# Performance work log

Hardware: AMD Instinct MI355X
Metric: run time of the kernel (lower is better)

## Reference

```python
import jax, jax.numpy as jnp
import numpy as np
from jax import lax

M, T, WINDOW = 4096, 2048, 25
NEG_DIAG = -1e10  # matches alphas.fill_diagonal_(-1e10)


def setup_inputs() -> dict:
    key = jax.random.key(0)
    k_ys, k_a, k_r, k_b0, k_b1 = jax.random.split(key, 5)
    ys = jax.random.uniform(k_ys, (M, T), dtype=jnp.float32) * 10.0  # case counts
    alphas = 0.01 * jax.random.normal(k_a, (M, M), dtype=jnp.float32)
    repro = 1.0 + 0.01 * jax.random.normal(k_r, (M, WINDOW), dtype=jnp.float32)  # init ones
    b0 = 0.1 * jax.random.normal(k_b0, (M, 1), dtype=jnp.float32)
    b1 = 0.01 * jax.random.normal(k_b1, (M, 1), dtype=jnp.float32)
    t = jnp.arange(T, dtype=jnp.int32) + 1
    return {"ys": ys, "alphas": alphas, "repro": repro, "b0": b0, "b1": b1, "t": t}


def reference(ys, alphas, repro, b0, b1, t):
    m, _ = ys.shape
    window = repro.shape[1]
    offset = window - 1
    # metapopulation weights: sigmoid adjacency with diagonal forced to ~0
    diag = jnp.eye(m, dtype=bool)
    W = jax.nn.sigmoid(jnp.where(diag, jnp.asarray(NEG_DIAG, ys.dtype), alphas))
    # depthwise conv1d (cross-correlation), groups=M, VALID padding -> (M, T-window+1)
    Z = lax.conv_general_dilated(
        ys[None],                 # (1, M, T)
        repro[:, None, :],        # (M, 1, window)
        window_strides=(1,),
        padding='VALID',
        feature_group_count=m,
        dimension_numbers=('NCH', 'OIH', 'NCH'),
    )[0]                          # (M, T')
    ys_n = ys[:, offset:]         # (M, T')
    # beta_net: per-node softplus-linear in time -> (M, T), then narrow
    tt = t.astype(ys.dtype)
    beta = jax.nn.softplus(b0 + b1 * tt[None, :])[:, offset:]  # (M, T')
    return beta * (jax.nn.softplus(Z) + W @ ys_n)
```

## Files before the change

### kernel.cpp

```cpp
#include <hip/hip_runtime.h>
#include <stdint.h>

#define M_DIM 4096
#define T_DIM 2048
#define N_OUT 2024
#define N_PAD 2048
#define WIN   25
#define K_DIM 4096

typedef float f32x4 __attribute__((ext_vector_type(4)));

__device__ __forceinline__ unsigned short f2bf(float x) {
  unsigned u = __float_as_uint(x);
  u += 0x7FFF + ((u >> 16) & 1);
  return (unsigned short)(u >> 16);
}
__device__ __forceinline__ float bf2f(unsigned short h) {
  return __uint_as_float(((unsigned)h) << 16);
}

__device__ __forceinline__ void gl2lds16(const void* g, void* l) {
  __builtin_amdgcn_global_load_lds(
      (const __attribute__((address_space(1))) unsigned int*)g,
      (__attribute__((address_space(3))) unsigned int*)l, 16, 0, 0);
}

__device__ __forceinline__ int pk_fp8x4(float a, float b, float c, float d) {
  int w = __builtin_amdgcn_cvt_pk_fp8_f32(a, b, 0, false);
  w = __builtin_amdgcn_cvt_pk_fp8_f32(c, d, w, true);
  return w;
}

__global__ __launch_bounds__(256) void k_wcast(const float* __restrict__ alphas,
                                               unsigned char* __restrict__ W8) {
  size_t i8 = ((size_t)blockIdx.x * 256 + threadIdx.x) * 8;
  const float4 v0 = *(const float4*)(alphas + i8);
  const float4 v1 = *(const float4*)(alphas + i8 + 4);
  int row = (int)(i8 >> 12);
  int col = (int)(i8 & 4095);
  float a[8] = {v0.x, v0.y, v0.z, v0.w, v1.x, v1.y, v1.z, v1.w};
  float w[8];
#pragma unroll
  for (int j = 0; j < 8; ++j)
    w[j] = (row == col + j) ? 0.f : 1.f / (1.f + __expf(-a[j]));
  int p0 = pk_fp8x4(w[0], w[1], w[2], w[3]);
  int p1 = pk_fp8x4(w[4], w[5], w[6], w[7]);
  *(uint2*)(W8 + i8) = uint2{(unsigned)p0, (unsigned)p1};
}

__global__ __launch_bounds__(256) void k_convT(const float* __restrict__ ys,
                                               const float* __restrict__ repro,
                                               unsigned short* __restrict__ Sbf,
                                               unsigned char* __restrict__ BT8) {
  __shared__ float sy[32][284];
  __shared__ float sr[32][26];
  const int tid = threadIdx.x;
  const int c0 = blockIdx.x * 256;
  const int m0 = blockIdx.y * 32;

  for (int slot = tid; slot < 32 * 70; slot += 256) {
    int r = slot / 70, f = slot % 70;
    int c = c0 + f * 4;
    float4 v = (c < T_DIM) ? *(const float4*)(ys + (size_t)(m0 + r) * T_DIM + c)
                           : float4{0.f, 0.f, 0.f, 0.f};
    sy[r][f * 4 + 0] = v.x; sy[r][f * 4 + 1] = v.y;
    sy[r][f * 4 + 2] = v.z; sy[r][f * 4 + 3] = v.w;
  }
  for (int slot = tid; slot < 32 * WIN; slot += 256) {
    int r = slot / WIN, k = slot % WIN;
    sr[r][k] = repro[(m0 + r) * WIN + k];
  }
  __syncthreads();

  {
    const int r = tid >> 3;
    const int cbase = (tid & 7) * 32;
    float y[56];
#pragma unroll
    for (int i = 0; i < 56; ++i) y[i] = sy[r][cbase + i];
    float rv[WIN];
#pragma unroll
    for (int k = 0; k < WIN; ++k) rv[k] = sr[r][k];
    unsigned pk[16];
#pragma unroll
    for (int jj = 0; jj < 32; ++jj) {
      float z = 0.f;
#pragma unroll
      for (int k = 0; k < WIN; ++k) z += y[jj + k] * rv[k];
      float sp = fmaxf(z, 0.f) + log1pf(__expf(-fabsf(z)));
      int gj = c0 + cbase + jj;
      unsigned short h = (gj < N_OUT) ? f2bf(sp) : (unsigned short)0;
      if (jj & 1) pk[jj >> 1] |= ((unsigned)h) << 16;
      else        pk[jj >> 1]  = (unsigned)h;
    }
    unsigned short* dst = Sbf + (size_t)(m0 + r) * N_PAD + c0 + cbase;
    *(uint4*)(dst)      = *(const uint4*)(pk + 0);
    *(uint4*)(dst + 8)  = *(const uint4*)(pk + 4);
    *(uint4*)(dst + 16) = *(const uint4*)(pk + 8);
    *(uint4*)(dst + 24) = *(const uint4*)(pk + 12);
  }

  {
    const int n = c0 + tid;
    const bool ok = (n < N_OUT);
    unsigned w[8];
#pragma unroll
    for (int i = 0; i < 8; ++i) {
      float a0 = ok ? sy[4 * i + 0][tid + 24] : 0.f;
      float a1 = ok ? sy[4 * i + 1][tid + 24] : 0.f;
      float a2 = ok ? sy[4 * i + 2][tid + 24] : 0.f;
      float a3 = ok ? sy[4 * i + 3][tid + 24] : 0.f;
      w[i] = (unsigned)pk_fp8x4(a0, a1, a2, a3);
    }
    unsigned char* dst = BT8 + (size_t)n * K_DIM + m0;
    *(uint4*)(dst)      = uint4{w[0], w[1], w[2], w[3]};
    *(uint4*)(dst + 16) = uint4{w[4], w[5], w[6], w[7]};
  }
}

__global__ __launch_bounds__(512, 4) void k_gemm(const unsigned char* __restrict__ W8,
                                                 const unsigned char* __restrict__ BT8,
                                                 const unsigned short* __restrict__ Sbf,
                                                 const float* __restrict__ b0,
                                                 const float* __restrict__ b1,
                                                 float* __restrict__ out) {
  __shared__ __align__(64) unsigned char lA[4][128 * 64];
  __shared__ __align__(64) unsigned char lB[4][128 * 64];
  const int tid  = threadIdx.x;
  const int wave = tid >> 6;
  const int lane = tid & 63;
  const int wm = wave >> 2;
  const int wn = wave & 3;
  const int m16  = lane & 15;
  const int quad = lane >> 4;

  const int fid  = blockIdx.y * gridDim.x + blockIdx.x;
  const int swz  = (fid & 7) * 64 + (fid >> 3);
  const int tileN = (swz & 15) * 128;
  const int tileM = (swz >> 4) * 128;

  const int key  = (m16 >> 1) & 3;
  const int sub  = (quad & 1) * 8;
  const int rowA = (wm * 64 + m16) * 64;
  const int rowB = (wn * 32 + m16) * 64;
  int hOf[2];
#pragma unroll
  for (int h = 0; h < 2; ++h)
    hOf[h] = (((2 * h + (quad >> 1)) ^ key) << 4) + sub;

  const int o = wave * 1024 + lane * 16;
  const int r = o >> 6;
  const int s = (o >> 4) & 3;
  const int q = s ^ ((r >> 1) & 3);
  const unsigned char* gA = W8  + (size_t)(tileM + r) * K_DIM + q * 16;
  const unsigned char* gB = BT8 + (size_t)(tileN + r) * K_DIM + q * 16;
  const int ldsOff = wave * 1024;

  f32x4 acc[4][2];
#pragma unroll
  for (int i = 0; i < 4; ++i)
#pragma unroll
    for (int j = 0; j < 2; ++j) acc[i][j] = f32x4{0.f, 0.f, 0.f, 0.f};

  auto stage = [&](int buf, int kt_) {
    const size_t kb_ = (size_t)kt_ * 64;
    gl2lds16(gA + kb_, &lA[buf][ldsOff]);
    gl2lds16(gB + kb_, &lB[buf][ldsOff]);
  };
  auto compute = [&](int buf) {
#pragma unroll
    for (int h = 0; h < 2; ++h) {
      long long aF[4], bF[2];
#pragma unroll
      for (int i = 0; i < 4; ++i)
        aF[i] = *(const long long*)&lA[buf][rowA + i * 1024 + hOf[h]];
#pragma unroll
      for (int j = 0; j < 2; ++j)
        bF[j] = *(const long long*)&lB[buf][rowB + j * 1024 + hOf[h]];
#pragma unroll
      for (int i = 0; i < 4; ++i)
#pragma unroll
        for (int j = 0; j < 2; ++j)
          acc[i][j] = __builtin_amdgcn_mfma_f32_16x16x32_fp8_fp8(
              aF[i], bF[j], acc[i][j], 0, 0, 0);
    }
  };

  stage(0, 0);
  stage(1, 1);
  stage(2, 2);

#pragma unroll 1
  for (int kt = 0; kt < K_DIM / 64; kt += 4) {
    stage(3, kt + 3);
    asm volatile("s_waitcnt vmcnt(6)" ::: "memory");
    __builtin_amdgcn_s_barrier();
    asm volatile("" ::: "memory");
    compute(0);
    __builtin_amdgcn_s_barrier();
    asm volatile("" ::: "memory");

    if (kt + 4 < K_DIM / 64) {
      stage(0, kt + 4);
      asm volatile("s_waitcnt vmcnt(6)" ::: "memory");
    } else {
      asm volatile("s_waitcnt vmcnt(4)" ::: "memory");
    }
    __builtin_amdgcn_s_barrier();
    asm volatile("" ::: "memory");
    compute(1);
    __builtin_amdgcn_s_barrier();
    asm volatile("" ::: "memory");

    if (kt + 5 < K_DIM / 64) {
      stage(1, kt + 5);
      asm volatile("s_waitcnt vmcnt(6)" ::: "memory");
    } else {
      asm volatile("s_waitcnt vmcnt(2)" ::: "memory");
    }
    __builtin_amdgcn_s_barrier();
    asm volatile("" ::: "memory");
    compute(2);
    __builtin_amdgcn_s_barrier();
    asm volatile("" ::: "memory");

    if (kt + 6 < K_DIM / 64) {
      stage(2, kt + 6);
      asm volatile("s_waitcnt vmcnt(6)" ::: "memory");
    } else {
      asm volatile("s_waitcnt vmcnt(0)" ::: "memory");
    }
    __builtin_amdgcn_s_barrier();
    asm volatile("" ::: "memory");
    compute(3);
    __builtin_amdgcn_s_barrier();
    asm volatile("" ::: "memory");
  }

#pragma unroll
  for (int j = 0; j < 2; ++j) {
    int gn = tileN + wn * 32 + j * 16 + m16;
    if (gn >= N_OUT) continue;
    float tval = (float)(gn + WIN);
#pragma unroll
    for (int i = 0; i < 4; ++i) {
#pragma unroll
      for (int r2 = 0; r2 < 4; ++r2) {
        int gm = tileM + wm * 64 + i * 16 + quad * 4 + r2;
        float x = b0[gm] + b1[gm] * tval;
        float beta = fmaxf(x, 0.f) + log1pf(__expf(-fabsf(x)));
        float sv = bf2f(Sbf[(size_t)gm * N_PAD + gn]);
        out[(size_t)gm * N_OUT + gn] = beta * (sv + acc[i][j][r2]);
      }
    }
  }
}

extern "C" void kernel_launch(void* const* d_in, const int* in_sizes, int n_in,
                              void* d_out, int out_size, void* d_ws, size_t ws_size,
                              hipStream_t stream) {
  const float* ys     = (const float*)d_in[0];
  const float* alphas = (const float*)d_in[1];
  const float* repro  = (const float*)d_in[2];
  const float* b0     = (const float*)d_in[3];
  const float* b1     = (const float*)d_in[4];
  float* out = (float*)d_out;

  char* ws = (char*)d_ws;
  unsigned char*  W8  = (unsigned char*)ws;
  unsigned char*  BT8 = (unsigned char*)(ws + (size_t)M_DIM * K_DIM);
  unsigned short* Sbf = (unsigned short*)(ws + (size_t)M_DIM * K_DIM
                                             + (size_t)N_PAD * K_DIM);

  k_wcast<<<(M_DIM * (size_t)K_DIM) / 8 / 256, 256, 0, stream>>>(alphas, W8);
  k_convT<<<dim3(T_DIM / 256, M_DIM / 32), 256, 0, stream>>>(ys, repro, Sbf, BT8);
  k_gemm<<<dim3(N_PAD / 128, M_DIM / 128), 512, 0, stream>>>(W8, BT8, Sbf,
                                                             b0, b1, out);
}
```

Baseline: 253.9 us.

## Enlarge FP8 GEMM tile to 256x128 with 1024-thread blocks and double buffering

```diff
diff --git a/kernel.cpp b/kernel.cpp
--- a/kernel.cpp
+++ b/kernel.cpp
@@ -118,14 +118,14 @@
   }
 }
 
-__global__ __launch_bounds__(512, 4) void k_gemm(const unsigned char* __restrict__ W8,
-                                                 const unsigned char* __restrict__ BT8,
-                                                 const unsigned short* __restrict__ Sbf,
-                                                 const float* __restrict__ b0,
-                                                 const float* __restrict__ b1,
-                                                 float* __restrict__ out) {
-  __shared__ __align__(64) unsigned char lA[4][128 * 64];
-  __shared__ __align__(64) unsigned char lB[4][128 * 64];
+__global__ __launch_bounds__(1024, 4) void k_gemm(const unsigned char* __restrict__ W8,
+                                                  const unsigned char* __restrict__ BT8,
+                                                  const unsigned short* __restrict__ Sbf,
+                                                  const float* __restrict__ b0,
+                                                  const float* __restrict__ b1,
+                                                  float* __restrict__ out) {
+  __shared__ __align__(64) unsigned char lA[2][256 * 64];
+  __shared__ __align__(64) unsigned char lB[2][128 * 64];
   const int tid  = threadIdx.x;
   const int wave = tid >> 6;
   const int lane = tid & 63;
@@ -135,9 +135,9 @@
   const int quad = lane >> 4;
 
   const int fid  = blockIdx.y * gridDim.x + blockIdx.x;
-  const int swz  = (fid & 7) * 64 + (fid >> 3);
+  const int swz  = (fid & 7) * 32 + (fid >> 3);
   const int tileN = (swz & 15) * 128;
-  const int tileM = (swz >> 4) * 128;
+  const int tileM = (swz >> 4) * 256;
 
   const int key  = (m16 >> 1) & 3;
   const int sub  = (quad & 1) * 8;
@@ -148,13 +148,15 @@
   for (int h = 0; h < 2; ++h)
     hOf[h] = (((2 * h + (quad >> 1)) ^ key) << 4) + sub;
 
-  const int o = wave * 1024 + lane * 16;
-  const int r = o >> 6;
-  const int s = (o >> 4) & 3;
-  const int q = s ^ ((r >> 1) & 3);
-  const unsigned char* gA = W8  + (size_t)(tileM + r) * K_DIM + q * 16;
-  const unsigned char* gB = BT8 + (size_t)(tileN + r) * K_DIM + q * 16;
-  const int ldsOff = wave * 1024;
+  const int oA = tid * 16;
+  const int rA = oA >> 6;
+  const int sA = (oA >> 4) & 3;
+  const int qA = sA ^ ((rA >> 1) & 3);
+  const unsigned char* gA = W8 + (size_t)(tileM + rA) * K_DIM + qA * 16;
+  const int rB = (tid * 16) >> 6;
+  const int qB = (((tid * 16) >> 4) & 3) ^ ((rB >> 1) & 3);
+  const unsigned char* gB = BT8 + (size_t)(tileN + rB) * K_DIM + qB * 16;
+  const int ldsBase = wave * 1024;
 
   f32x4 acc[4][2];
 #pragma unroll
@@ -164,8 +166,8 @@
 
   auto stage = [&](int buf, int kt_) {
     const size_t kb_ = (size_t)kt_ * 64;
-    gl2lds16(gA + kb_, &lA[buf][ldsOff]);
-    gl2lds16(gB + kb_, &lB[buf][ldsOff]);
+    gl2lds16(gA + kb_, &lA[buf][ldsBase]);
+    if (wave < 8) gl2lds16(gB + kb_, &lB[buf][ldsBase]);
   };
   auto compute = [&](int buf) {
 #pragma unroll
@@ -187,52 +189,34 @@
   };
 
   stage(0, 0);
-  stage(1, 1);
-  stage(2, 2);
 
 #pragma unroll 1
-  for (int kt = 0; kt < K_DIM / 64; kt += 4) {
-    stage(3, kt + 3);
-    asm volatile("s_waitcnt vmcnt(6)" ::: "memory");
+  for (int kt = 0; kt < K_DIM / 64; kt += 2) {
+    stage(1, kt + 1);
+    if (wave < 8) {
+      asm volatile("s_waitcnt vmcnt(2)" ::: "memory");
+    } else {
+      asm volatile("s_waitcnt vmcnt(1)" ::: "memory");
+    }
     __builtin_amdgcn_s_barrier();
     asm volatile("" ::: "memory");
     compute(0);
     __builtin_amdgcn_s_barrier();
     asm volatile("" ::: "memory");
 
-    if (kt + 4 < K_DIM / 64) {
-      stage(0, kt + 4);
-      asm volatile("s_waitcnt vmcnt(6)" ::: "memory");
-    } else {
-      asm volatile("s_waitcnt vmcnt(4)" ::: "memory");
-    }
-    __builtin_amdgcn_s_barrier();
-    asm volatile("" ::: "memory");
-    compute(1);
-    __builtin_amdgcn_s_barrier();
-    asm volatile("" ::: "memory");
-
-    if (kt + 5 < K_DIM / 64) {
-      stage(1, kt + 5);
-      asm volatile("s_waitcnt vmcnt(6)" ::: "memory");
-    } else {
-      asm volatile("s_waitcnt vmcnt(2)" ::: "memory");
-    }
-    __builtin_amdgcn_s_barrier();
-    asm volatile("" ::: "memory");
-    compute(2);
-    __builtin_amdgcn_s_barrier();
-    asm volatile("" ::: "memory");
-
-    if (kt + 6 < K_DIM / 64) {
-      stage(2, kt + 6);
-      asm volatile("s_waitcnt vmcnt(6)" ::: "memory");
+    if (kt + 2 < K_DIM / 64) {
+      stage(0, kt + 2);
+      if (wave < 8) {
+        asm volatile("s_waitcnt vmcnt(2)" ::: "memory");
+      } else {
+        asm volatile("s_waitcnt vmcnt(1)" ::: "memory");
+      }
     } else {
       asm volatile("s_waitcnt vmcnt(0)" ::: "memory");
     }
     __builtin_amdgcn_s_barrier();
     asm volatile("" ::: "memory");
-    compute(3);
+    compute(1);
     __builtin_amdgcn_s_barrier();
     asm volatile("" ::: "memory");
   }
@@ -274,6 +258,6 @@
 
   k_wcast<<<(M_DIM * (size_t)K_DIM) / 8 / 256, 256, 0, stream>>>(alphas, W8);
   k_convT<<<dim3(T_DIM / 256, M_DIM / 32), 256, 0, stream>>>(ys, repro, Sbf, BT8);
-  k_gemm<<<dim3(N_PAD / 128, M_DIM / 128), 512, 0, stream>>>(W8, BT8, Sbf,
-                                                             b0, b1, out);
-}
+  k_gemm<<<dim3(N_PAD / 128, M_DIM / 256), 1024, 0, stream>>>(W8, BT8, Sbf,
+                                                              b0, b1, out);
+}
```

New measurement: 263.0 us. 3.6% more time.
